# Kernel optimization log

Hardware: AMD Instinct MI355X
Metric: run time of the kernel (lower is better)

Reference implementation:

```python
import jax, jax.numpy as jnp
import numpy as np

N = 100000      # nodes
E = 1600000     # edges (before self-loops)
IN_DIM = 128
HID = 32
HEADS = 4
EMB = 128
SLOPE = 0.2     # PyG GATConv default negative_slope


def setup_inputs() -> dict:
    key = jax.random.key(0)
    ks = jax.random.split(key, 16)
    def glorot(k, shape):
        fan_in = shape[0] if len(shape) > 1 else shape[-1]
        return jax.random.normal(k, shape, jnp.float32) * (1.0 / np.sqrt(fan_in))
    x = jax.random.normal(ks[0], (N, IN_DIM), jnp.float32)
    edge_index = jax.random.randint(ks[1], (2, E), 0, N)
    return {
        "x": x,
        "edge_index": edge_index,
        # layer 1: in_dim -> hidden (heads=4, concat)
        "W1": glorot(ks[2], (IN_DIM, HEADS * HID)),
        "att_src1": glorot(ks[3], (HEADS, HID)),
        "att_dst1": glorot(ks[4], (HEADS, HID)),
        "b1": jnp.zeros((HEADS * HID,), jnp.float32),
        # layer 2: hidden*heads -> hidden (heads=4, concat)
        "W2": glorot(ks[5], (HEADS * HID, HEADS * HID)),
        "att_src2": glorot(ks[6], (HEADS, HID)),
        "att_dst2": glorot(ks[7], (HEADS, HID)),
        "b2": jnp.zeros((HEADS * HID,), jnp.float32),
        # layer 3: hidden*heads -> embed (heads=1)
        "W3": glorot(ks[8], (HEADS * HID, EMB)),
        "att_src3": glorot(ks[9], (1, EMB)),
        "att_dst3": glorot(ks[10], (1, EMB)),
        "b3": jnp.zeros((EMB,), jnp.float32),
    }


def gat_conv(x, src, dst, W, att_src, att_dst, b, heads, out_ch):
    """One PyG-style GATConv (concat=True). src/dst already include self-loops."""
    n = x.shape[0]
    h = (x @ W).reshape(n, heads, out_ch)                 # [N,H,C]
    a_s = jnp.einsum('nhc,hc->nh', h, att_src)            # [N,H]
    a_d = jnp.einsum('nhc,hc->nh', h, att_dst)            # [N,H]
    e = jax.nn.leaky_relu(a_s[src] + a_d[dst], SLOPE)     # [E',H]
    # numerically stable softmax over irregular incoming neighborhoods (per dst)
    m = jax.ops.segment_max(e, dst, num_segments=n)       # [N,H]
    ex = jnp.exp(e - m[dst])
    denom = jax.ops.segment_sum(ex, dst, num_segments=n)  # [N,H]
    alpha = ex / denom[dst]                                # [E',H]
    out = jax.ops.segment_sum(h[src] * alpha[:, :, None], dst, num_segments=n)
    return out.reshape(n, heads * out_ch) + b


def reference(x, edge_index, W1, att_src1, att_dst1, b1,
              W2, att_src2, att_dst2, b2, W3, att_src3, att_dst3, b3):
    n = x.shape[0]
    loops = jnp.arange(n, dtype=edge_index.dtype)
    src = jnp.concatenate([edge_index[0], loops])  # PyG add_self_loops=True
    dst = jnp.concatenate([edge_index[1], loops])
    h = gat_conv(x, src, dst, W1, att_src1, att_dst1, b1, HEADS, HID)
    h = jax.nn.elu(h)
    h = gat_conv(h, src, dst, W2, att_src2, att_dst2, b2, HEADS, HID)
    h = jax.nn.elu(h)
    out = gat_conv(h, src, dst, W3, att_src3, att_dst3, b3, 1, EMB)
    return out
```

## Files before the change

kernel.cpp:

```cpp
#include <hip/hip_runtime.h>
#include <hip/hip_fp16.h>
#include <math.h>

#define N_NODES 100000
#define N_EDGES 1600000
#define SLOPE 0.2f

#define BSHIFT 8
#define NB 391
#define CHUNK 8192

typedef _Float16 f16x8 __attribute__((ext_vector_type(8)));
typedef float f32x4 __attribute__((ext_vector_type(4)));
typedef float f32x8v __attribute__((ext_vector_type(8)));

__global__ __launch_bounds__(256) void partA1(const int* __restrict__ ei,
                                              int* __restrict__ bucket_count,
                                              int E, int n) {
  __shared__ int cnt[NB];
  for (int i = threadIdx.x; i < NB; i += 256) cnt[i] = 0;
  __syncthreads();
  int base = blockIdx.x * CHUNK;
  int total = E + n;
  int lim = min(base + CHUNK, total);
  for (int e = base + threadIdx.x; e < lim; e += 256) {
    int d = (e < E) ? ei[E + e] : (e - E);
    atomicAdd(&cnt[d >> BSHIFT], 1);
  }
  __syncthreads();
  for (int i = threadIdx.x; i < NB; i += 256)
    if (cnt[i]) atomicAdd(&bucket_count[i], cnt[i]);
}

__global__ __launch_bounds__(512) void scan_nb(
    const int* __restrict__ bucket_count, int* __restrict__ bucket_base,
    int* __restrict__ bucket_cursor) {
  __shared__ int lds[512];
  int t = threadIdx.x;
  int v = (t < NB) ? bucket_count[t] : 0;
  int x = v;
  lds[t] = x;
  __syncthreads();
  for (int off = 1; off < 512; off <<= 1) {
    int y = (t >= off) ? lds[t - off] : 0;
    __syncthreads();
    x += y;
    lds[t] = x;
    __syncthreads();
  }
  int excl = x - v;
  if (t <= NB) bucket_base[t] = excl;
  if (t < NB) bucket_cursor[t] = excl;
}

__global__ __launch_bounds__(256) void partA2(const int* __restrict__ ei,
                                              int* __restrict__ bucket_cursor,
                                              unsigned* __restrict__ part,
                                              int E, int n) {
  __shared__ int cnt[NB];
  __shared__ int res[NB];
  for (int i = threadIdx.x; i < NB; i += 256) cnt[i] = 0;
  __syncthreads();
  int base = blockIdx.x * CHUNK;
  int total = E + n;
  int lim = min(base + CHUNK, total);
  for (int e = base + threadIdx.x; e < lim; e += 256) {
    int d = (e < E) ? ei[E + e] : (e - E);
    atomicAdd(&cnt[d >> BSHIFT], 1);
  }
  __syncthreads();
  for (int i = threadIdx.x; i < NB; i += 256)
    res[i] = cnt[i] ? atomicAdd(&bucket_cursor[i], cnt[i]) : 0;
  __syncthreads();
  for (int e = base + threadIdx.x; e < lim; e += 256) {
    int s, d;
    if (e < E) { s = ei[e]; d = ei[E + e]; } else { s = d = e - E; }
    int b = d >> BSHIFT;
    int pos = atomicAdd(&res[b], 1);
    part[pos] = ((unsigned)s << BSHIFT) | (unsigned)(d & 255);
  }
}

__global__ __launch_bounds__(256) void passB(const unsigned* __restrict__ part,
                                             const int* __restrict__ bucket_base,
                                             int* __restrict__ row_start,
                                             int* __restrict__ edge_src, int n) {
  __shared__ int cnt[256];
  __shared__ int sc[256];
  __shared__ int loff[256];
  int b = blockIdx.x;
  int t = threadIdx.x;
  int node0 = b << BSHIFT;
  int bstart = bucket_base[b], bend = bucket_base[b + 1];
  cnt[t] = 0;
  __syncthreads();
  for (int i = bstart + t; i < bend; i += 256)
    atomicAdd(&cnt[part[i] & 255], 1);
  __syncthreads();
  int v = cnt[t];
  int x = v;
  sc[t] = x;
  __syncthreads();
  for (int off = 1; off < 256; off <<= 1) {
    int y = (t >= off) ? sc[t - off] : 0;
    __syncthreads();
    x += y;
    sc[t] = x;
    __syncthreads();
  }
  int excl = x - v;
  loff[t] = excl;
  int node = node0 + t;
  if (node < n) row_start[node] = bstart + excl;
  if (b == NB - 1 && t == 0) row_start[n] = bucket_base[NB];
  __syncthreads();
  for (int i = bstart + t; i < bend; i += 256) {
    unsigned p = part[i];
    int dl = p & 255;
    int pos = bstart + atomicAdd(&loff[dl], 1);
    edge_src[pos] = (int)(p >> BSHIFT);
  }
}

__global__ __launch_bounds__(256) void convert_w(
    const float* __restrict__ W1, const float* __restrict__ W2,
    const float* __restrict__ W3, __half* __restrict__ Wt1,
    __half* __restrict__ Wt2, __half* __restrict__ Wt3) {
  int idx = blockIdx.x * 256 + threadIdx.x;
  if (idx >= 3 * 16384) return;
  int mat = idx >> 14;
  int r = idx & 16383;
  int k = r >> 7, col = r & 127;
  const float* W = (mat == 0) ? W1 : (mat == 1) ? W2 : W3;
  __half* Wt = (mat == 0) ? Wt1 : (mat == 1) ? Wt2 : Wt3;
  Wt[col * 128 + k] = __float2half(W[k * 128 + col]);
}

template <int H, typename InT>
__global__ __launch_bounds__(256, 4) void gemm_att_mfma(
    const InT* __restrict__ X, const __half* __restrict__ Wt,
    const float* __restrict__ att_src, const float* __restrict__ att_dst,
    __half* __restrict__ Y, float* __restrict__ a_s, float* __restrict__ a_d,
    int n) {
  __shared__ _Float16 B_lds[128 * 128];
  int t = threadIdx.x;
  int r0 = blockIdx.x * 64;
  int wv = t >> 6, lane = t & 63, quad = lane >> 4, l15 = lane & 15;

  {
    const __half* wp = Wt + t * 64;
    int brow = t >> 1;
    int sbase = (t & 1) * 8;
#pragma unroll
    for (int i = 0; i < 8; i++) {
      int slot = (sbase + i) ^ (brow & 15);
      *(float4*)&B_lds[brow * 128 + slot * 8] = *(const float4*)(wp + i * 8);
    }
  }

  int arow = r0 + wv * 16 + l15;
  bool inb = arow < n;
  f16x8 a[4];
  if constexpr (sizeof(InT) == 4) {
    const float* xp = (const float*)X + (size_t)arow * 128 + quad * 8;
#pragma unroll
    for (int kb = 0; kb < 4; kb++) {
      float4 v0, v1;
      if (inb) {
        v0 = *(const float4*)(xp + kb * 32);
        v1 = *(const float4*)(xp + kb * 32 + 4);
      } else {
        v0 = make_float4(0.f, 0.f, 0.f, 0.f);
        v1 = v0;
      }
      f32x8v f = {v0.x, v0.y, v0.z, v0.w, v1.x, v1.y, v1.z, v1.w};
      a[kb] = __builtin_convertvector(f, f16x8);
    }
  } else {
    const __half* xp = (const __half*)X + (size_t)arow * 128 + quad * 8;
    f16x8 z = {};
#pragma unroll
    for (int kb = 0; kb < 4; kb++) {
      if (inb) a[kb] = *(const f16x8*)(xp + kb * 32);
      else a[kb] = z;
    }
  }
  __syncthreads();

  f32x4 acc[8];
#pragma unroll
  for (int ct = 0; ct < 8; ct++) acc[ct] = (f32x4){0.f, 0.f, 0.f, 0.f};

#pragma unroll
  for (int kb = 0; kb < 4; kb++) {
#pragma unroll
    for (int ct = 0; ct < 8; ct++) {
      f16x8 b = *(const f16x8*)(
          &B_lds[(ct * 16 + l15) * 128 + (((kb * 4 + quad) ^ l15) * 8)]);
      acc[ct] = __builtin_amdgcn_mfma_f32_16x16x32_f16(a[kb], b, acc[ct], 0, 0, 0);
    }
  }

  int rbase = r0 + wv * 16 + quad * 4;
#pragma unroll
  for (int reg = 0; reg < 4; reg++) {
    int row = rbase + reg;
    if (row < n) {
#pragma unroll
      for (int ct = 0; ct < 8; ct++)
        Y[(size_t)row * 128 + ct * 16 + l15] = __float2half(acc[ct][reg]);
    }
  }

  float avs[8], avd[8];
#pragma unroll
  for (int ct = 0; ct < 8; ct++) {
    avs[ct] = att_src[ct * 16 + l15];
    avd[ct] = att_dst[ct * 16 + l15];
  }
  if constexpr (H == 4) {
    float ps[4][4], pd_[4][4];
#pragma unroll
    for (int hd = 0; hd < 4; hd++)
#pragma unroll
      for (int reg = 0; reg < 4; reg++) { ps[hd][reg] = 0.f; pd_[hd][reg] = 0.f; }
#pragma unroll
    for (int ct = 0; ct < 8; ct++) {
      int hd = ct >> 1;
#pragma unroll
      for (int reg = 0; reg < 4; reg++) {
        ps[hd][reg] = fmaf(acc[ct][reg], avs[ct], ps[hd][reg]);
        pd_[hd][reg] = fmaf(acc[ct][reg], avd[ct], pd_[hd][reg]);
      }
    }
#pragma unroll
    for (int off = 1; off <= 8; off <<= 1)
#pragma unroll
      for (int hd = 0; hd < 4; hd++)
#pragma unroll
        for (int reg = 0; reg < 4; reg++) {
          ps[hd][reg] += __shfl_xor(ps[hd][reg], off, 64);
          pd_[hd][reg] += __shfl_xor(pd_[hd][reg], off, 64);
        }
#pragma unroll
    for (int hd = 0; hd < 4; hd++)
      if (l15 == hd) {
#pragma unroll
        for (int reg = 0; reg < 4; reg++) {
          int row = rbase + reg;
          if (row < n) {
            a_s[row * 4 + hd] = ps[hd][reg];
            a_d[row * 4 + hd] = pd_[hd][reg];
          }
        }
      }
  } else {
    float ps[4] = {}, pd_[4] = {};
#pragma unroll
    for (int ct = 0; ct < 8; ct++)
#pragma unroll
      for (int reg = 0; reg < 4; reg++) {
        ps[reg] = fmaf(acc[ct][reg], avs[ct], ps[reg]);
        pd_[reg] = fmaf(acc[ct][reg], avd[ct], pd_[reg]);
      }
#pragma unroll
    for (int off = 1; off <= 8; off <<= 1)
#pragma unroll
      for (int reg = 0; reg < 4; reg++) {
        ps[reg] += __shfl_xor(ps[reg], off, 64);
        pd_[reg] += __shfl_xor(pd_[reg], off, 64);
      }
    if (l15 == 0) {
#pragma unroll
      for (int reg = 0; reg < 4; reg++) {
        int row = rbase + reg;
        if (row < n) { a_s[row] = ps[reg]; a_d[row] = pd_[reg]; }
      }
    }
  }
}

template <int H, bool DO_ELU, typename OutT>
__global__ __launch_bounds__(256) void agg_kernel(
    const __half* __restrict__ h, const float* __restrict__ a_s,
    const float* __restrict__ a_d, const int* __restrict__ row_start,
    const int* __restrict__ edge_src, const float* __restrict__ bias,
    OutT* __restrict__ out, int n) {
  const int C = 128 / H;
  __shared__ float w_lds[4][H * 66];
  __shared__ int sn_lds[4][64];
  int wslot = threadIdx.x >> 6;
  int wid = (blockIdx.x * blockDim.x + threadIdx.x) >> 6;
  int lane = threadIdx.x & 63;
  if (wid >= n) return;
  int start = row_start[wid], end = row_start[wid + 1];
  int deg = end - start;

  float adv[H];
#pragma unroll
  for (int hh = 0; hh < H; hh++) adv[hh] = a_d[wid * H + hh];

  if (deg <= 64) {
    bool valid = lane < deg;
    int sn = valid ? edge_src[start + lane] : 0;
    float e[H];
    if (valid) {
      if constexpr (H == 4) {
        float4 asv = *(const float4*)(a_s + (size_t)sn * 4);
        float t0 = asv.x + adv[0];
        float t1 = asv.y + adv[1];
        float t2 = asv.z + adv[2];
        float t3 = asv.w + adv[3];
        e[0] = t0 >= 0.f ? t0 : SLOPE * t0;
        e[1] = t1 >= 0.f ? t1 : SLOPE * t1;
        e[2] = t2 >= 0.f ? t2 : SLOPE * t2;
        e[3] = t3 >= 0.f ? t3 : SLOPE * t3;
      } else {
        float tt = a_s[sn] + adv[0];
        e[0] = tt >= 0.f ? tt : SLOPE * tt;
      }
    } else {
#pragma unroll
      for (int hh = 0; hh < H; hh++) e[hh] = -1e30f;
    }
    bool small = (deg <= 32);
    float w[H], s[H];
#pragma unroll
    for (int hh = 0; hh < H; hh++) {
      w[hh] = valid ? __expf(e[hh] - 40.f) : 0.f;
      s[hh] = w[hh];
    }
#pragma unroll
    for (int off = 1; off <= 16; off <<= 1)
#pragma unroll
      for (int hh = 0; hh < H; hh++) s[hh] += __shfl_xor(s[hh], off, 64);
    if (!small)
#pragma unroll
      for (int hh = 0; hh < H; hh++) s[hh] += __shfl_xor(s[hh], 32, 64);
    sn_lds[wslot][lane] = sn << 8;
#pragma unroll
    for (int hh = 0; hh < H; hh++)
      w_lds[wslot][hh * 66 + lane] = valid ? w[hh] * (1.f / s[hh]) : 0.f;
    __builtin_amdgcn_wave_barrier();

    int g = lane >> 4, l = lane & 15;
    int d0 = l * 8;
    const char* hb = (const char*)h + l * 16;
    int headBase = (H == 4) ? (l >> 2) * 66 : 0;
    f32x8v acc = {};
    int degp16 = (deg + 15) & ~15;
    for (int eidx = 0; eidx < degp16; eidx += 16) {
#pragma unroll
      for (int jj = 0; jj < 4; jj++) {
        int ei2 = eidx + jj * 4 + g;
        int boff = sn_lds[wslot][ei2];
        float wv = w_lds[wslot][headBase + ei2];
        f16x8 hv = *(const f16x8*)(hb + (unsigned)boff);
        f32x8v pf = __builtin_convertvector(hv, f32x8v);
        f32x8v ws = {wv, wv, wv, wv, wv, wv, wv, wv};
        acc = pf * ws + acc;
      }
    }
    float o[8];
#pragma unroll
    for (int k = 0; k < 8; k++) {
      float v = acc[k];
      v += __shfl_xor(v, 16, 64);
      v += __shfl_xor(v, 32, 64);
      o[k] = v;
    }
    if (lane < 16) {
      float4 bv0 = *(const float4*)(bias + d0);
      float4 bv1 = *(const float4*)(bias + d0 + 4);
      o[0] += bv0.x; o[1] += bv0.y; o[2] += bv0.z; o[3] += bv0.w;
      o[4] += bv1.x; o[5] += bv1.y; o[6] += bv1.z; o[7] += bv1.w;
      if (DO_ELU) {
#pragma unroll
        for (int k = 0; k < 8; k++)
          o[k] = (o[k] > 0.f) ? o[k] : __expf(o[k]) - 1.f;
      }
      if constexpr (sizeof(OutT) == 2) {
        union { float4 f4; __half2 h2[4]; } uo;
        uo.h2[0] = __floats2half2_rn(o[0], o[1]);
        uo.h2[1] = __floats2half2_rn(o[2], o[3]);
        uo.h2[2] = __floats2half2_rn(o[4], o[5]);
        uo.h2[3] = __floats2half2_rn(o[6], o[7]);
        *(float4*)((__half*)out + (size_t)wid * 128 + d0) = uo.f4;
      } else {
        float4 ov0 = {o[0], o[1], o[2], o[3]};
        float4 ov1 = {o[4], o[5], o[6], o[7]};
        *(float4*)((float*)out + (size_t)wid * 128 + d0) = ov0;
        *(float4*)((float*)out + (size_t)wid * 128 + d0 + 4) = ov1;
      }
    }
    return;
  }

  {
    const int G = C / 2;
    int head = lane / G;
    float m[H], s[H];
#pragma unroll
    for (int hh = 0; hh < H; hh++) { m[hh] = -1e30f; s[hh] = 0.f; }
    for (int idx = start + lane; idx < end; idx += 64) {
      int sn = edge_src[idx];
#pragma unroll
      for (int hh = 0; hh < H; hh++) {
        float e = a_s[sn * H + hh] + adv[hh];
        e = (e >= 0.f) ? e : SLOPE * e;
        float mn = fmaxf(m[hh], e);
        s[hh] = s[hh] * __expf(m[hh] - mn) + __expf(e - mn);
        m[hh] = mn;
      }
    }
    for (int off = 1; off < 64; off <<= 1) {
#pragma unroll
      for (int hh = 0; hh < H; hh++) {
        float mo = __shfl_xor(m[hh], off, 64);
        float so = __shfl_xor(s[hh], off, 64);
        float mn = fmaxf(m[hh], mo);
        s[hh] = s[hh] * __expf(m[hh] - mn) + so * __expf(mo - mn);
        m[hh] = mn;
      }
    }
    int d0 = lane * 2;
    float mh = m[head];
    float rsh = 1.f / s[head];
    float adh = adv[head];
    float acc0 = 0.f, acc1 = 0.f;
    for (int idx = start; idx < end; idx++) {
      int sn = edge_src[idx];
      float e = a_s[sn * H + head] + adh;
      e = (e >= 0.f) ? e : SLOPE * e;
      float w = __expf(e - mh) * rsh;
      float2 hv = __half22float2(*(const __half2*)(h + (size_t)sn * 128 + d0));
      acc0 += w * hv.x;
      acc1 += w * hv.y;
    }
    float o0 = acc0 + bias[d0];
    float o1 = acc1 + bias[d0 + 1];
    if (DO_ELU) {
      o0 = (o0 > 0.f) ? o0 : __expf(o0) - 1.f;
      o1 = (o1 > 0.f) ? o1 : __expf(o1) - 1.f;
    }
    out[(size_t)wid * 128 + d0] = (OutT)o0;
    out[(size_t)wid * 128 + d0 + 1] = (OutT)o1;
  }
}

extern "C" void kernel_launch(void* const* d_in, const int* in_sizes, int n_in,
                              void* d_out, int out_size, void* d_ws,
                              size_t ws_size, hipStream_t stream) {
  const float* x = (const float*)d_in[0];
  const int* ei = (const int*)d_in[1];
  const float* W1 = (const float*)d_in[2];
  const float* as1 = (const float*)d_in[3];
  const float* ad1 = (const float*)d_in[4];
  const float* b1 = (const float*)d_in[5];
  const float* W2 = (const float*)d_in[6];
  const float* as2 = (const float*)d_in[7];
  const float* ad2 = (const float*)d_in[8];
  const float* b2 = (const float*)d_in[9];
  const float* W3 = (const float*)d_in[10];
  const float* as3 = (const float*)d_in[11];
  const float* ad3 = (const float*)d_in[12];
  const float* b3 = (const float*)d_in[13];
  float* out = (float*)d_out;

  const int n = N_NODES, E = N_EDGES, total = E + n;

  char* ws = (char*)d_ws;
  size_t off = 0;
  auto alloc = [&](size_t bytes) -> char* {
    char* p = ws + off;
    off = (off + bytes + 255) & ~(size_t)255;
    return p;
  };
  __half* hbuf = (__half*)alloc(sizeof(__half) * (size_t)n * 128);
  float* a_s = (float*)alloc(sizeof(float) * n * 4);
  float* a_d = (float*)alloc(sizeof(float) * n * 4);
  unsigned* part = (unsigned*)alloc(sizeof(unsigned) * total);
  int* edge_src = (int*)alloc(sizeof(int) * total);
  int* row_start = (int*)alloc(sizeof(int) * (n + 1));
  int* bucket_count = (int*)alloc(sizeof(int) * (NB + 1));
  int* bucket_base = (int*)alloc(sizeof(int) * (NB + 1));
  int* bucket_cursor = (int*)alloc(sizeof(int) * (NB + 1));
  __half* Wt1 = (__half*)alloc(sizeof(__half) * 16384);
  __half* Wt2 = (__half*)alloc(sizeof(__half) * 16384);
  __half* Wt3 = (__half*)alloc(sizeof(__half) * 16384);
  __half* hbuf2 = (__half*)alloc(sizeof(__half) * (size_t)n * 128);
  bool fp16mid = (off <= ws_size);

  hipMemsetAsync(bucket_count, 0, sizeof(int) * (NB + 1), stream);

  convert_w<<<192, 256, 0, stream>>>(W1, W2, W3, Wt1, Wt2, Wt3);

  int nblkA = (total + CHUNK - 1) / CHUNK;
  partA1<<<nblkA, 256, 0, stream>>>(ei, bucket_count, E, n);
  scan_nb<<<1, 512, 0, stream>>>(bucket_count, bucket_base, bucket_cursor);
  partA2<<<nblkA, 256, 0, stream>>>(ei, bucket_cursor, part, E, n);
  passB<<<NB, 256, 0, stream>>>(part, bucket_base, row_start, edge_src, n);

  int agg_blocks = (n + 3) / 4;
  int gemm_blocks = (n + 63) / 64;

  if (fp16mid) {
    gemm_att_mfma<4, float><<<gemm_blocks, 256, 0, stream>>>(
        x, Wt1, as1, ad1, hbuf, a_s, a_d, n);
    agg_kernel<4, true, __half><<<agg_blocks, 256, 0, stream>>>(
        hbuf, a_s, a_d, row_start, edge_src, b1, hbuf2, n);

    gemm_att_mfma<4, __half><<<gemm_blocks, 256, 0, stream>>>(
        hbuf2, Wt2, as2, ad2, hbuf, a_s, a_d, n);
    agg_kernel<4, true, __half><<<agg_blocks, 256, 0, stream>>>(
        hbuf, a_s, a_d, row_start, edge_src, b2, hbuf2, n);

    gemm_att_mfma<1, __half><<<gemm_blocks, 256, 0, stream>>>(
        hbuf2, Wt3, as3, ad3, hbuf, a_s, a_d, n);
    agg_kernel<1, false, float><<<agg_blocks, 256, 0, stream>>>(
        hbuf, a_s, a_d, row_start, edge_src, b3, out, n);
  } else {
    gemm_att_mfma<4, float><<<gemm_blocks, 256, 0, stream>>>(
        x, Wt1, as1, ad1, hbuf, a_s, a_d, n);
    agg_kernel<4, true, float><<<agg_blocks, 256, 0, stream>>>(
        hbuf, a_s, a_d, row_start, edge_src, b1, out, n);

    gemm_att_mfma<4, float><<<gemm_blocks, 256, 0, stream>>>(
        out, Wt2, as2, ad2, hbuf, a_s, a_d, n);
    agg_kernel<4, true, float><<<agg_blocks, 256, 0, stream>>>(
        hbuf, a_s, a_d, row_start, edge_src, b2, out, n);

    gemm_att_mfma<1, float><<<gemm_blocks, 256, 0, stream>>>(
        out, Wt3, as3, ad3, hbuf, a_s, a_d, n);
    agg_kernel<1, false, float><<<agg_blocks, 256, 0, stream>>>(
        hbuf, a_s, a_d, row_start, edge_src, b3, out, n);
  }
}
```

Before: 466.4 us.

## Precompute per-block bucket offsets and stage GEMM output through LDS

The partition pass now saves per-block bucket counts in partA1 and adds a per-bucket scan kernel that produces deterministic per-block write offsets. partA2 no longer re-reads the destination indices or performs global atomic reservations. Separately, the GEMM epilogue writes its fp16 results into LDS first and then stores full 16-byte row segments instead of scattered 2-byte writes. The cost is an extra small kernel launch, extra workspace for the block-count tables, and a barrier in the GEMM epilogue.

New measurement: 457.1 us. 2.0% less time.

```diff
diff --git a/kernel.cpp b/kernel.cpp
--- a/kernel.cpp
+++ b/kernel.cpp
@@ -16,11 +16,13 @@
 
 __global__ __launch_bounds__(256) void partA1(const int* __restrict__ ei,
                                               int* __restrict__ bucket_count,
-                                              int E, int n) {
+                                              int* __restrict__ blkcnt,
+                                              int E, int n, int nblk) {
   __shared__ int cnt[NB];
   for (int i = threadIdx.x; i < NB; i += 256) cnt[i] = 0;
   __syncthreads();
-  int base = blockIdx.x * CHUNK;
+  int b = blockIdx.x;
+  int base = b * CHUNK;
   int total = E + n;
   int lim = min(base + CHUNK, total);
   for (int e = base + threadIdx.x; e < lim; e += 256) {
@@ -28,13 +30,15 @@
     atomicAdd(&cnt[d >> BSHIFT], 1);
   }
   __syncthreads();
-  for (int i = threadIdx.x; i < NB; i += 256)
-    if (cnt[i]) atomicAdd(&bucket_count[i], cnt[i]);
+  for (int i = threadIdx.x; i < NB; i += 256) {
+    int c = cnt[i];
+    blkcnt[i * nblk + b] = c;
+    if (c) atomicAdd(&bucket_count[i], c);
+  }
 }
 
 __global__ __launch_bounds__(512) void scan_nb(
-    const int* __restrict__ bucket_count, int* __restrict__ bucket_base,
-    int* __restrict__ bucket_cursor) {
+    const int* __restrict__ bucket_count, int* __restrict__ bucket_base) {
   __shared__ int lds[512];
   int t = threadIdx.x;
   int v = (t < NB) ? bucket_count[t] : 0;
@@ -50,33 +54,44 @@
   }
   int excl = x - v;
   if (t <= NB) bucket_base[t] = excl;
-  if (t < NB) bucket_cursor[t] = excl;
+}
+
+__global__ __launch_bounds__(256) void scan_blk(
+    const int* __restrict__ blkcnt, const int* __restrict__ bucket_base,
+    int* __restrict__ blk_base, int nblk) {
+  __shared__ int lds[256];
+  int i = blockIdx.x;
+  int t = threadIdx.x;
+  int v = (t < nblk) ? blkcnt[i * nblk + t] : 0;
+  int x = v;
+  lds[t] = x;
+  __syncthreads();
+  for (int off = 1; off < 256; off <<= 1) {
+    int y = (t >= off) ? lds[t - off] : 0;
+    __syncthreads();
+    x += y;
+    lds[t] = x;
+    __syncthreads();
+  }
+  if (t < nblk) blk_base[i * nblk + t] = bucket_base[i] + (x - v);
 }
 
 __global__ __launch_bounds__(256) void partA2(const int* __restrict__ ei,
-                                              int* __restrict__ bucket_cursor,
+                                              const int* __restrict__ blk_base,
                                               unsigned* __restrict__ part,
-                                              int E, int n) {
-  __shared__ int cnt[NB];
+                                              int E, int n, int nblk) {
   __shared__ int res[NB];
-  for (int i = threadIdx.x; i < NB; i += 256) cnt[i] = 0;
-  __syncthreads();
-  int base = blockIdx.x * CHUNK;
+  int b = blockIdx.x;
+  for (int i = threadIdx.x; i < NB; i += 256) res[i] = blk_base[i * nblk + b];
+  __syncthreads();
+  int base = b * CHUNK;
   int total = E + n;
   int lim = min(base + CHUNK, total);
   for (int e = base + threadIdx.x; e < lim; e += 256) {
-    int d = (e < E) ? ei[E + e] : (e - E);
-    atomicAdd(&cnt[d >> BSHIFT], 1);
-  }
-  __syncthreads();
-  for (int i = threadIdx.x; i < NB; i += 256)
-    res[i] = cnt[i] ? atomicAdd(&bucket_cursor[i], cnt[i]) : 0;
-  __syncthreads();
-  for (int e = base + threadIdx.x; e < lim; e += 256) {
     int s, d;
     if (e < E) { s = ei[e]; d = ei[E + e]; } else { s = d = e - E; }
-    int b = d >> BSHIFT;
-    int pos = atomicAdd(&res[b], 1);
+    int bk = d >> BSHIFT;
+    int pos = atomicAdd(&res[bk], 1);
     part[pos] = ((unsigned)s << BSHIFT) | (unsigned)(d & 255);
   }
 }
@@ -202,15 +217,6 @@
   }
 
   int rbase = r0 + wv * 16 + quad * 4;
-#pragma unroll
-  for (int reg = 0; reg < 4; reg++) {
-    int row = rbase + reg;
-    if (row < n) {
-#pragma unroll
-      for (int ct = 0; ct < 8; ct++)
-        Y[(size_t)row * 128 + ct * 16 + l15] = __float2half(acc[ct][reg]);
-    }
-  }
 
   float avs[8], avd[8];
 #pragma unroll
@@ -275,6 +281,29 @@
       for (int reg = 0; reg < 4; reg++) {
         int row = rbase + reg;
         if (row < n) { a_s[row] = ps[reg]; a_d[row] = pd_[reg]; }
+      }
+    }
+  }
+
+  __syncthreads();
+  {
+    const int LW = 136;
+    _Float16* wreg = &B_lds[wv * 16 * LW];
+#pragma unroll
+    for (int reg = 0; reg < 4; reg++) {
+      int rl = quad * 4 + reg;
+#pragma unroll
+      for (int ct = 0; ct < 8; ct++)
+        wreg[rl * LW + ct * 16 + l15] = (_Float16)acc[ct][reg];
+    }
+#pragma unroll
+    for (int j = 0; j < 4; j++) {
+      int rl = j * 4 + (lane >> 4);
+      int seg = lane & 15;
+      int rowg = r0 + wv * 16 + rl;
+      if (rowg < n) {
+        float4 v = *(const float4*)&wreg[rl * LW + seg * 8];
+        *(float4*)(Y + (size_t)rowg * 128 + seg * 8) = v;
       }
     }
   }
@@ -468,6 +497,7 @@
   float* out = (float*)d_out;
 
   const int n = N_NODES, E = N_EDGES, total = E + n;
+  const int nblkA = (total + CHUNK - 1) / CHUNK;
 
   char* ws = (char*)d_ws;
   size_t off = 0;
@@ -484,7 +514,8 @@
   int* row_start = (int*)alloc(sizeof(int) * (n + 1));
   int* bucket_count = (int*)alloc(sizeof(int) * (NB + 1));
   int* bucket_base = (int*)alloc(sizeof(int) * (NB + 1));
-  int* bucket_cursor = (int*)alloc(sizeof(int) * (NB + 1));
+  int* blkcnt = (int*)alloc(sizeof(int) * NB * nblkA);
+  int* blk_base = (int*)alloc(sizeof(int) * NB * nblkA);
   __half* Wt1 = (__half*)alloc(sizeof(__half) * 16384);
   __half* Wt2 = (__half*)alloc(sizeof(__half) * 16384);
   __half* Wt3 = (__half*)alloc(sizeof(__half) * 16384);
@@ -495,10 +526,10 @@
 
   convert_w<<<192, 256, 0, stream>>>(W1, W2, W3, Wt1, Wt2, Wt3);
 
-  int nblkA = (total + CHUNK - 1) / CHUNK;
-  partA1<<<nblkA, 256, 0, stream>>>(ei, bucket_count, E, n);
-  scan_nb<<<1, 512, 0, stream>>>(bucket_count, bucket_base, bucket_cursor);
-  partA2<<<nblkA, 256, 0, stream>>>(ei, bucket_cursor, part, E, n);
+  partA1<<<nblkA, 256, 0, stream>>>(ei, bucket_count, blkcnt, E, n, nblkA);
+  scan_nb<<<1, 512, 0, stream>>>(bucket_count, bucket_base);
+  scan_blk<<<NB, 256, 0, stream>>>(blkcnt, bucket_base, blk_base, nblkA);
+  partA2<<<nblkA, 256, 0, stream>>>(ei, blk_base, part, E, n, nblkA);
   passB<<<NB, 256, 0, stream>>>(part, bucket_base, row_start, edge_src, n);
 
   int agg_blocks = (n + 3) / 4;
```
